# Performance work log

Hardware: AMD Instinct MI355X
Metric: run time of the kernel (lower is better)

The kernel has to match this reference:

```python
import jax, jax.numpy as jnp
import numpy as np

NUM_TEAMS = 200000
EMBED_DIM = 16
NUM_EDGES = 3200000
BATCH = 500000
EPS_NORM = 1e-12  # F.normalize clamp
EPS_SOFTMAX = 1e-16  # PyG edge-softmax denom eps
NEG_SLOPE = 0.01  # LeakyReLU default


def setup_inputs() -> dict:
    key = jax.random.key(0)
    ks = jax.random.split(key, 12)
    inp = {}
    inp["embed"] = jax.random.normal(ks[0], (NUM_TEAMS, EMBED_DIM), dtype=jnp.float32)
    inp["beta"] = jnp.ones((2,), dtype=jnp.float32)  # one learnable scalar per AGNNConv
    # torch Linear init ~ U(-1/sqrt(fan_in), 1/sqrt(fan_in)); stored as [in, out]
    def lin(k, fi, fo):
        b = 1.0 / np.sqrt(fi)
        k1, k2 = jax.random.split(k)
        return (jax.random.uniform(k1, (fi, fo), jnp.float32, -b, b),
                jax.random.uniform(k2, (fo,), jnp.float32, -b, b))
    inp["lin0_w"], inp["lin0_b"] = lin(ks[1], 2 * EMBED_DIM, 6)
    inp["lin1_w"], inp["lin1_b"] = lin(ks[2], 6, 16)
    inp["lin2_w"], inp["lin2_b"] = lin(ks[3], 16, 3)
    inp["edge_index"] = jax.random.randint(ks[4], (2, NUM_EDGES), 0, NUM_TEAMS, dtype=jnp.int64)
    inp["home"] = jax.random.randint(ks[5], (BATCH,), 0, NUM_TEAMS, dtype=jnp.int64)
    inp["away"] = jax.random.randint(ks[6], (BATCH,), 0, NUM_TEAMS, dtype=jnp.int64)
    return inp


def _agnn_conv(x, beta, src, dst, n):
    # x: [N, D]; messages flow src(j) -> dst(i); scatter-softmax over edges per dst
    xn = x / jnp.maximum(jnp.linalg.norm(x, axis=-1, keepdims=True), EPS_NORM)
    alpha = beta * jnp.sum(xn[src] * xn[dst], axis=-1)          # [E]
    m = jax.ops.segment_max(alpha, dst, num_segments=n)          # [N]
    a = jnp.exp(alpha - m[dst])                                   # [E]
    denom = jax.ops.segment_sum(a, dst, num_segments=n)          # [N]
    a = a / (denom[dst] + EPS_SOFTMAX)
    return jax.ops.segment_sum(a[:, None] * x[src], dst, num_segments=n)  # [N, D]


def _forward(embed, beta, lin0_w, lin0_b, lin1_w, lin1_b, lin2_w, lin2_b,
             src, dst, home, away):
    n = embed.shape[0]
    act = lambda v: jax.nn.leaky_relu(v, NEG_SLOPE)
    x = embed  # embedding of arange(n_teams) == the table itself
    x = act(_agnn_conv(x, beta[0], src, dst, n))
    x = act(_agnn_conv(x, beta[1], src, dst, n))
    h = jnp.concatenate([x[home], x[away]], axis=-1)  # [B, 2D]
    h = act(h @ lin0_w + lin0_b)
    h = act(h @ lin1_w + lin1_b)
    h = act(h @ lin2_w + lin2_b)
    return jax.nn.log_softmax(h, axis=0).reshape(-1, 3)  # LogSoftmax(dim=0), faithful


def reference(embed, beta, lin0_w, lin0_b, lin1_w, lin1_b, lin2_w, lin2_b,
              edge_index, home, away):
    n = embed.shape[0]
    # AGNNConv default: remove then add self-loops
    loops = jnp.arange(n, dtype=edge_index.dtype)
    mask = edge_index[0] != edge_index[1]
    safe = jnp.where(mask, edge_index[1], edge_index[0])  # self-loop-out non-loop edges
    src = jnp.concatenate([edge_index[0], loops])
    dst = jnp.concatenate([jnp.where(mask, edge_index[1], edge_index[0]), loops])
    # masked self-loops in original list become src==dst duplicates of the appended
    # self-loops only if random collision; to faithfully *remove* them we redirect
    # removed edges onto the node's own appended self-loop (alpha identical for
    # src==dst), which changes only duplicate self-loop counts with prob ~1/N.
    return _forward(embed, beta, lin0_w, lin0_b, lin1_w, lin1_b, lin2_w, lin2_b,
                    src, dst, home, away)
```

## Files before the change

### kernel.cpp

```cpp
#include <hip/hip_runtime.h>
#include <hip/hip_fp16.h>
#include <math.h>

#define TPB 256
#define NPB 512
#define NPB_SHIFT 9
#define EPB 8192
#define EPW 16
#define BCAP 12288

typedef float v2f __attribute__((ext_vector_type(2)));

__device__ __forceinline__ float leaky_relu(float v) { return v > 0.0f ? v : 0.01f * v; }

__device__ __forceinline__ float dot4(float4 a, float4 b) {
    return a.x * b.x + a.y * b.y + a.z * b.z + a.w * b.w;
}
__device__ __forceinline__ float4 f4_scale(float4 a, float s) {
    return make_float4(a.x * s, a.y * s, a.z * s, a.w * s);
}
__device__ __forceinline__ float4 f4_acc(float4 a, float w, float4 y) {
    return make_float4(fmaf(w, y.x, a.x), fmaf(w, y.y, a.y),
                       fmaf(w, y.z, a.z), fmaf(w, y.w, a.w));
}
__device__ __forceinline__ float4 f4_add_shfl(float4 v, int d) {
    return make_float4(v.x + __shfl_xor(v.x, d, 64), v.y + __shfl_xor(v.y, d, 64),
                       v.z + __shfl_xor(v.z, d, 64), v.w + __shfl_xor(v.w, d, 64));
}
__device__ __forceinline__ float4 leaky4(float4 v) {
    return make_float4(leaky_relu(v.x), leaky_relu(v.y), leaky_relu(v.z), leaky_relu(v.w));
}

__device__ __forceinline__ float4 dec4(unsigned w) {
    v2f lo = __builtin_amdgcn_cvt_pk_f32_fp8((int)w, false);
    v2f hi = __builtin_amdgcn_cvt_pk_f32_fp8((int)w, true);
    return make_float4(lo.x, lo.y, hi.x, hi.y);
}
__device__ __forceinline__ unsigned enc4(float4 v) {
    int r = __builtin_amdgcn_cvt_pk_fp8_f32(v.x, v.y, 0, false);
    r = __builtin_amdgcn_cvt_pk_fp8_f32(v.z, v.w, r, true);
    return (unsigned)r;
}

__device__ __forceinline__ void store_h4(__half* row, int l, float4 v) {
    union { float2 f; __half h[4]; } u;
    u.h[0] = __float2half(v.x); u.h[1] = __float2half(v.y);
    u.h[2] = __float2half(v.z); u.h[3] = __float2half(v.w);
    ((float2*)row)[l] = u.f;
}

__device__ __forceinline__ int wave_incl_scan(int v, int lane) {
#pragma unroll
    for (int off = 1; off < 64; off <<= 1) {
        int u = __shfl_up(v, off, 64);
        if (lane >= off) v += u;
    }
    return v;
}

__global__ void k_binA(const int* __restrict__ src, const int* __restrict__ dst,
                       unsigned* __restrict__ bdata, int* __restrict__ cbase,
                       int* __restrict__ ccnt, int E, int K,
                       const float* __restrict__ x, uint4* __restrict__ xq,
                       int N) {
    __shared__ int hist[512];
    __shared__ unsigned lcol[EPB];
    __shared__ int wsum[8];
    int t = threadIdx.x;
    int lane = t & 63, wv = t >> 6;
    int c = blockIdx.x;
    int e0 = c * EPB;
    int e1 = min(e0 + EPB, E);
    int tot = e1 - e0;
    hist[t] = 0;
    __syncthreads();
    int myd[EPW], mys[EPW];
    if (tot == EPB) {
        const int4* d4 = (const int4*)(dst + e0);
        const int4* s4 = (const int4*)(src + e0);
#pragma unroll
        for (int k = 0; k < 4; ++k) {
            int4 dd = d4[t + k * 512];
            int4 ss = s4[t + k * 512];
            myd[4 * k + 0] = dd.x; myd[4 * k + 1] = dd.y;
            myd[4 * k + 2] = dd.z; myd[4 * k + 3] = dd.w;
            mys[4 * k + 0] = ss.x; mys[4 * k + 1] = ss.y;
            mys[4 * k + 2] = ss.z; mys[4 * k + 3] = ss.w;
            atomicAdd(&hist[dd.x >> NPB_SHIFT], 1);
            atomicAdd(&hist[dd.y >> NPB_SHIFT], 1);
            atomicAdd(&hist[dd.z >> NPB_SHIFT], 1);
            atomicAdd(&hist[dd.w >> NPB_SHIFT], 1);
        }
    } else {
#pragma unroll
        for (int k = 0; k < EPW; ++k) {
            int e = e0 + t + k * 512;
            int d = (e < e1) ? dst[e] : -1;
            mys[k] = (e < e1) ? src[e] : 0;
            myd[k] = d;
            if (d >= 0) atomicAdd(&hist[d >> NPB_SHIFT], 1);
        }
    }
    __syncthreads();
    int v = hist[t];
    int inc = wave_incl_scan(v, lane);
    if (lane == 63) wsum[wv] = inc;
    __syncthreads();
    if (t == 0) {
        int acc = 0;
#pragma unroll
        for (int k = 0; k < 8; ++k) { int xv = wsum[k]; wsum[k] = acc; acc += xv; }
    }
    __syncthreads();
    int excl = inc + wsum[wv] - v;
    if (t < K) {
        cbase[(size_t)c * K + t] = excl;
        ccnt[(size_t)c * K + t] = v;
    }
    __syncthreads();
    hist[t] = excl;
    __syncthreads();
    if (tot == EPB) {
#pragma unroll
        for (int k = 0; k < EPW; ++k) {
            int d = myd[k];
            int p = atomicAdd(&hist[d >> NPB_SHIFT], 1);
            lcol[p] = ((unsigned)(d & (NPB - 1)) << 18) | (unsigned)mys[k];
        }
    } else {
#pragma unroll
        for (int k = 0; k < EPW; ++k) {
            int d = myd[k];
            if (d >= 0) {
                int p = atomicAdd(&hist[d >> NPB_SHIFT], 1);
                lcol[p] = ((unsigned)(d & (NPB - 1)) << 18) | (unsigned)mys[k];
            }
        }
    }
    __syncthreads();
    unsigned* outp = bdata + (size_t)c * EPB;
    for (int i = t; i < tot; i += 512) outp[i] = lcol[i];
    int i = c * 512 + t;
    if (i < N) {
        const float4* xp = (const float4*)(x + (size_t)i * 16);
        float4 a = xp[0], b = xp[1], cc = xp[2], d = xp[3];
        xq[i] = make_uint4(enc4(a), enc4(b), enc4(cc), enc4(d));
    }
}

__global__ void k_binB(const unsigned* __restrict__ bdata, const int* __restrict__ cbase,
                       const int* __restrict__ ccnt,
                       int2* __restrict__ rng,
                       int* __restrict__ col, int N, int NC, int K) {
    __shared__ int cb[512];
    __shared__ int cc[512];
    __shared__ int ldeg[NPB];
    __shared__ int wsum[8];
    int b = blockIdx.x, t = threadIdx.x;
    int lane = t & 63, wv = t >> 6;
    int n0 = b << NPB_SHIFT;
    int nn = min(NPB, N - n0);
    cb[t] = (t < NC) ? cbase[(size_t)t * K + b] : 0;
    cc[t] = (t < NC) ? ccnt[(size_t)t * K + b] : 0;
    ldeg[t] = 0;
    __syncthreads();
    int mycnt = (t < NC) ? cc[t] : 0;
    const unsigned* myp = bdata + (size_t)t * EPB + cb[t];
    for (int k = 0; k < mycnt; ++k) {
        unsigned e = myp[k];
        atomicAdd(&ldeg[e >> 18], 1);
    }
    __syncthreads();
    int dv = ldeg[t];
    int inc = wave_incl_scan(dv, lane);
    if (lane == 63) wsum[wv] = inc;
    __syncthreads();
    if (t == 0) {
        int acc = 0;
#pragma unroll
        for (int k = 0; k < 8; ++k) { int xv = wsum[k]; wsum[k] = acc; acc += xv; }
    }
    __syncthreads();
    int excl = inc + wsum[wv] - dv;
    int gb = b * BCAP;
    if (t < nn) {
        rng[n0 + t] = make_int2(gb + excl, gb + excl + dv);
    }
    __syncthreads();
    ldeg[t] = excl;
    __syncthreads();
    for (int k = 0; k < mycnt; ++k) {
        unsigned e = myp[k];
        int pos = atomicAdd(&ldeg[e >> 18], 1);
        col[gb + pos] = (int)(e & 0x3FFFFu);
    }
}

__global__ void k_agnn(const uint4* __restrict__ xq,
                       const int2* __restrict__ rng,
                       const int* __restrict__ col,
                       const float* __restrict__ beta_ptr, int beta_idx,
                       void* __restrict__ out, int n, int fp8_out) {
    int t = threadIdx.x;
    int l = t & 7;
    int i = blockIdx.x * (512 / 8) + (t >> 3);
    if (i >= n) return;
    float bet = beta_ptr[beta_idx];
    uint4 rowi = xq[i];
    float4 x0 = dec4(rowi.x), x1 = dec4(rowi.y), x2 = dec4(rowi.z), x3 = dec4(rowi.w);
    float sqi = dot4(x0, x0) + dot4(x1, x1) + dot4(x2, x2) + dot4(x3, x3);
    float inv_ni = rsqrtf(fmaxf(sqi, 1e-24f));
    float bi = bet * inv_ni;
    float4 q0 = f4_scale(x0, bi), q1 = f4_scale(x1, bi),
           q2 = f4_scale(x2, bi), q3 = f4_scale(x3, bi);
    float s;
    float4 a0, a1, a2, a3;
    if (l == 0) {
        float w = __expf(bet);
        s = w;
        a0 = f4_scale(x0, w); a1 = f4_scale(x1, w);
        a2 = f4_scale(x2, w); a3 = f4_scale(x3, w);
    } else {
        s = 0.0f;
        a0 = a1 = a2 = a3 = make_float4(0.f, 0.f, 0.f, 0.f);
    }
    int2 se = rng[i];
    int e1 = se.y;
    int last = max(e1 - 1, 0);
    int e = se.x + l;
    int j0 = min(max(col[min(e, last)], 0), n - 1);
    uint4 rA = xq[j0];
    int j1 = min(max(col[min(e + 8, last)], 0), n - 1);
    uint4 rB = xq[j1];
    for (; e < e1; e += 8) {
        int j2 = min(max(col[min(e + 16, last)], 0), n - 1);
        uint4 rC = xq[j2];
        float4 y0 = dec4(rA.x), y1 = dec4(rA.y), y2 = dec4(rA.z), y3 = dec4(rA.w);
        float sq = dot4(y0, y0) + dot4(y1, y1) + dot4(y2, y2) + dot4(y3, y3);
        float inv_n = rsqrtf(fmaxf(sq, 1e-24f));
        float d = (dot4(y0, q0) + dot4(y1, q1) + dot4(y2, q2) + dot4(y3, q3)) * inv_n;
        float w = __expf(d);
        s += w;
        a0 = f4_acc(a0, w, y0);
        a1 = f4_acc(a1, w, y1);
        a2 = f4_acc(a2, w, y2);
        a3 = f4_acc(a3, w, y3);
        rA = rB; rB = rC;
    }
#pragma unroll
    for (int d_ = 1; d_ < 8; d_ <<= 1) {
        s += __shfl_xor(s, d_, 64);
        a0 = f4_add_shfl(a0, d_);
        a1 = f4_add_shfl(a1, d_);
        a2 = f4_add_shfl(a2, d_);
        a3 = f4_add_shfl(a3, d_);
    }
    float inv = 1.0f / (s + 1e-16f);
    float4 o0 = leaky4(f4_scale(a0, inv));
    float4 o1 = leaky4(f4_scale(a1, inv));
    float4 o2 = leaky4(f4_scale(a2, inv));
    float4 o3 = leaky4(f4_scale(a3, inv));
    if (l < 4) {
        float4 oq = (l == 0) ? o0 : (l == 1) ? o1 : (l == 2) ? o2 : o3;
        if (fp8_out) {
            ((unsigned*)((uint4*)out + i))[l] = enc4(oq);
        } else {
            store_h4((__half*)out + (size_t)i * 16, l, oq);
        }
    }
}

__global__ void k_mlp(const __half* __restrict__ x, const int* __restrict__ home,
                      const int* __restrict__ away,
                      const float* __restrict__ w0, const float* __restrict__ b0,
                      const float* __restrict__ w1, const float* __restrict__ b1,
                      const float* __restrict__ w2, const float* __restrict__ b2,
                      float* __restrict__ z, float* __restrict__ bmax,
                      float* __restrict__ bsum, int nb) {
    __shared__ float sw0[192], sw1[96], sw2[48], sb0[6], sb1[16], sb2[3];
    __shared__ float rmax[4][3];
    __shared__ float rsum[4][3];
    int t = threadIdx.x;
    if (t < 192) sw0[t] = w0[t];
    if (t < 96)  sw1[t] = w1[t];
    if (t < 48)  sw2[t] = w2[t];
    if (t < 6)   sb0[t] = b0[t];
    if (t < 16)  sb1[t] = b1[t];
    if (t < 3)   sb2[t] = b2[t];
    __syncthreads();
    int i = blockIdx.x * blockDim.x + t;
    bool act = i < nb;
    float z0 = -3.4e38f, z1 = -3.4e38f, z2 = -3.4e38f;
    if (act) {
        float h[32];
        const uint4* hr = (const uint4*)(x + (size_t)home[i] * 16);
        const uint4* ar = (const uint4*)(x + (size_t)away[i] * 16);
        uint4 hv0 = hr[0], hv1 = hr[1];
        uint4 av0 = ar[0], av1 = ar[1];
        union { uint4 u; __half2 h2[4]; } cv;
#pragma unroll
        for (int q = 0; q < 4; ++q) {
            cv.u = (q == 0) ? hv0 : (q == 1) ? hv1 : (q == 2) ? av0 : av1;
#pragma unroll
            for (int k = 0; k < 4; ++k) {
                float2 f = __half22float2(cv.h2[k]);
                h[q * 8 + 2 * k + 0] = f.x;
                h[q * 8 + 2 * k + 1] = f.y;
            }
        }
        float t0[6];
#pragma unroll
        for (int o = 0; o < 6; ++o) {
            float acc = sb0[o];
#pragma unroll
            for (int k = 0; k < 32; ++k) acc = fmaf(h[k], sw0[k * 6 + o], acc);
            t0[o] = leaky_relu(acc);
        }
        float t1[16];
#pragma unroll
        for (int o = 0; o < 16; ++o) {
            float acc = sb1[o];
#pragma unroll
            for (int k = 0; k < 6; ++k) acc = fmaf(t0[k], sw1[k * 16 + o], acc);
            t1[o] = leaky_relu(acc);
        }
        float zz[3];
#pragma unroll
        for (int o = 0; o < 3; ++o) {
            float acc = sb2[o];
#pragma unroll
            for (int k = 0; k < 16; ++k) acc = fmaf(t1[k], sw2[k * 3 + o], acc);
            zz[o] = leaky_relu(acc);
            z[(size_t)i * 3 + o] = zz[o];
        }
        z0 = zz[0]; z1 = zz[1]; z2 = zz[2];
    }
    float w0_ = z0, w1_ = z1, w2_ = z2;
#pragma unroll
    for (int off = 32; off > 0; off >>= 1) {
        w0_ = fmaxf(w0_, __shfl_down(w0_, off));
        w1_ = fmaxf(w1_, __shfl_down(w1_, off));
        w2_ = fmaxf(w2_, __shfl_down(w2_, off));
    }
    int wid = t >> 6;
    if ((t & 63) == 0) { rmax[wid][0] = w0_; rmax[wid][1] = w1_; rmax[wid][2] = w2_; }
    __syncthreads();
    float M0 = fmaxf(fmaxf(rmax[0][0], rmax[1][0]), fmaxf(rmax[2][0], rmax[3][0]));
    float M1 = fmaxf(fmaxf(rmax[0][1], rmax[1][1]), fmaxf(rmax[2][1], rmax[3][1]));
    float M2 = fmaxf(fmaxf(rmax[0][2], rmax[1][2]), fmaxf(rmax[2][2], rmax[3][2]));
    float e0 = act ? __expf(z0 - M0) : 0.0f;
    float e1 = act ? __expf(z1 - M1) : 0.0f;
    float e2 = act ? __expf(z2 - M2) : 0.0f;
#pragma unroll
    for (int off = 32; off > 0; off >>= 1) {
        e0 += __shfl_down(e0, off);
        e1 += __shfl_down(e1, off);
        e2 += __shfl_down(e2, off);
    }
    if ((t & 63) == 0) { rsum[wid][0] = e0; rsum[wid][1] = e1; rsum[wid][2] = e2; }
    __syncthreads();
    if (t == 0) {
        float S0 = rsum[0][0] + rsum[1][0] + rsum[2][0] + rsum[3][0];
        float S1 = rsum[0][1] + rsum[1][1] + rsum[2][1] + rsum[3][1];
        float S2 = rsum[0][2] + rsum[1][2] + rsum[2][2] + rsum[3][2];
        bmax[blockIdx.x * 3 + 0] = M0; bmax[blockIdx.x * 3 + 1] = M1; bmax[blockIdx.x * 3 + 2] = M2;
        bsum[blockIdx.x * 3 + 0] = S0; bsum[blockIdx.x * 3 + 1] = S1; bsum[blockIdx.x * 3 + 2] = S2;
    }
}

__device__ __forceinline__ float pick3(int c, float L0, float L1, float L2) {
    return c == 0 ? L0 : (c == 1 ? L1 : L2);
}

__global__ void k_final(const float4* __restrict__ z4,
                        const float* __restrict__ bmax, const float* __restrict__ bsum,
                        int nblk, float4* __restrict__ out4, int n4) {
    __shared__ float lm[4][3];
    __shared__ float ls[4][3];
    __shared__ float Lsh[3];
    int t = threadIdx.x;
    float M0 = -3.4e38f, M1 = -3.4e38f, M2 = -3.4e38f;
    float S0 = 0.f, S1 = 0.f, S2 = 0.f;
    for (int b = t; b < nblk; b += 256) {
        float m0 = bmax[b * 3 + 0], s0 = bsum[b * 3 + 0];
        float n0 = fmaxf(M0, m0); S0 = S0 * __expf(M0 - n0) + s0 * __expf(m0 - n0); M0 = n0;
        float m1 = bmax[b * 3 + 1], s1 = bsum[b * 3 + 1];
        float n1 = fmaxf(M1, m1); S1 = S1 * __expf(M1 - n1) + s1 * __expf(m1 - n1); M1 = n1;
        float m2 = bmax[b * 3 + 2], s2 = bsum[b * 3 + 2];
        float n2 = fmaxf(M2, m2); S2 = S2 * __expf(M2 - n2) + s2 * __expf(m2 - n2); M2 = n2;
    }
#pragma unroll
    for (int off = 32; off > 0; off >>= 1) {
        float mo, so, nm;
        mo = __shfl_down(M0, off); so = __shfl_down(S0, off);
        nm = fmaxf(M0, mo); S0 = S0 * __expf(M0 - nm) + so * __expf(mo - nm); M0 = nm;
        mo = __shfl_down(M1, off); so = __shfl_down(S1, off);
        nm = fmaxf(M1, mo); S1 = S1 * __expf(M1 - nm) + so * __expf(mo - nm); M1 = nm;
        mo = __shfl_down(M2, off); so = __shfl_down(S2, off);
        nm = fmaxf(M2, mo); S2 = S2 * __expf(M2 - nm) + so * __expf(mo - nm); M2 = nm;
    }
    int wid = t >> 6;
    if ((t & 63) == 0) {
        lm[wid][0] = M0; lm[wid][1] = M1; lm[wid][2] = M2;
        ls[wid][0] = S0; ls[wid][1] = S1; ls[wid][2] = S2;
    }
    __syncthreads();
    if (t == 0) {
        for (int w = 1; w < 4; ++w) {
            float nm;
            nm = fmaxf(M0, lm[w][0]); S0 = S0 * __expf(M0 - nm) + ls[w][0] * __expf(lm[w][0] - nm); M0 = nm;
            nm = fmaxf(M1, lm[w][1]); S1 = S1 * __expf(M1 - nm) + ls[w][1] * __expf(lm[w][1] - nm); M1 = nm;
            nm = fmaxf(M2, lm[w][2]); S2 = S2 * __expf(M2 - nm) + ls[w][2] * __expf(lm[w][2] - nm); M2 = nm;
        }
        Lsh[0] = M0 + logf(S0);
        Lsh[1] = M1 + logf(S1);
        Lsh[2] = M2 + logf(S2);
    }
    __syncthreads();
    float L0 = Lsh[0], L1 = Lsh[1], L2 = Lsh[2];
    int i = blockIdx.x * blockDim.x + t;
    if (i >= n4) return;
    float4 v = z4[i];
    int c = i % 3;
    int c1 = (c + 1) % 3, c2 = (c + 2) % 3;
    out4[i] = make_float4(v.x - pick3(c, L0, L1, L2),
                          v.y - pick3(c1, L0, L1, L2),
                          v.z - pick3(c2, L0, L1, L2),
                          v.w - pick3(c, L0, L1, L2));
}

extern "C" void kernel_launch(void* const* d_in, const int* in_sizes, int n_in,
                              void* d_out, int out_size, void* d_ws, size_t ws_size,
                              hipStream_t stream) {
    const float* embed = (const float*)d_in[0];
    const float* beta  = (const float*)d_in[1];
    const float* w0 = (const float*)d_in[2];
    const float* b0 = (const float*)d_in[3];
    const float* w1 = (const float*)d_in[4];
    const float* b1 = (const float*)d_in[5];
    const float* w2 = (const float*)d_in[6];
    const float* b2 = (const float*)d_in[7];
    const int* eidx = (const int*)d_in[8];
    const int* home = (const int*)d_in[9];
    const int* away = (const int*)d_in[10];

    const int N = in_sizes[0] / 16;
    const int E = in_sizes[8] / 2;
    const int B = in_sizes[9];
    const int* esrc = eidx;
    const int* edst = eidx + E;
    const int K = (N + NPB - 1) >> NPB_SHIFT;
    const int NC = (E + EPB - 1) / EPB;

    char* ws = (char*)d_ws;
    size_t off = 0;
    auto alloc = [&](size_t bytes) -> char* {
        off = (off + 255) & ~(size_t)255;
        char* p = ws + off;
        off += bytes;
        return p;
    };
    size_t bdata_bytes = (size_t)NC * EPB * 4;
    size_t alias_bytes = (((size_t)N * 16 + 511) & ~(size_t)255) + (size_t)B * 3 * 4;
    char* U = alloc(bdata_bytes > alias_bytes ? bdata_bytes : alias_bytes);
    unsigned* bdata = (unsigned*)U;
    uint4* xq1  = (uint4*)U;
    float* zbuf = (float*)(U + (((size_t)N * 16 + 511) & ~(size_t)255));

    int2* rng    = (int2*)alloc((size_t)N * 8);
    int* colw    = (int*)alloc((size_t)K * BCAP * 4);
    int* cbase   = (int*)alloc((size_t)NC * K * 4);
    int* ccnt    = (int*)alloc((size_t)NC * K * 4);
    uint4* xq0   = (uint4*)alloc((size_t)N * 16);
    __half* xh2  = (__half*)alloc((size_t)N * 32);
    const int nblkB = (B + TPB - 1) / TPB;
    float* bmax  = (float*)alloc((size_t)nblkB * 3 * 4);
    float* bsum  = (float*)alloc((size_t)nblkB * 3 * 4);
    (void)ws_size; (void)n_in; (void)out_size;

    k_binA<<<NC, 512, 0, stream>>>(esrc, edst, bdata, cbase, ccnt, E, K,
                                   embed, xq0, N);
    k_binB<<<K, 512, 0, stream>>>(bdata, cbase, ccnt, rng, colw, N, NC, K);

    const int nblkN8 = (N + 63) / 64;
    k_agnn<<<nblkN8, 512, 0, stream>>>(xq0, rng, colw, beta, 0, xq1, N, 1);
    k_agnn<<<nblkN8, 512, 0, stream>>>(xq1, rng, colw, beta, 1, xh2, N, 0);

    k_mlp<<<nblkB, TPB, 0, stream>>>(xh2, home, away, w0, b0, w1, b1, w2, b2,
                                     zbuf, bmax, bsum, B);
    const int n4 = (B * 3) / 4;
    k_final<<<(n4 + TPB - 1) / TPB, TPB, 0, stream>>>((const float4*)zbuf, bmax, bsum,
                                                      nblkB, (float4*)d_out, n4);
}
```

Before: 214.3 us.

## Coalesce bin-B reads per chunk and stage sorted columns in LDS

```diff
diff --git a/kernel.cpp b/kernel.cpp
--- a/kernel.cpp
+++ b/kernel.cpp
@@ -62,7 +62,7 @@
                        unsigned* __restrict__ bdata, int* __restrict__ cbase,
                        int* __restrict__ ccnt, int E, int K,
                        const float* __restrict__ x, uint4* __restrict__ xq,
-                       int N) {
+                       int N, int NC) {
     __shared__ int hist[512];
     __shared__ unsigned lcol[EPB];
     __shared__ int wsum[8];
@@ -114,8 +114,8 @@
     __syncthreads();
     int excl = inc + wsum[wv] - v;
     if (t < K) {
-        cbase[(size_t)c * K + t] = excl;
-        ccnt[(size_t)c * K + t] = v;
+        cbase[(size_t)t * NC + c] = excl;
+        ccnt[(size_t)t * NC + c] = v;
     }
     __syncthreads();
     hist[t] = excl;
@@ -152,27 +152,21 @@
                        const int* __restrict__ ccnt,
                        int2* __restrict__ rng,
                        int* __restrict__ col, int N, int NC, int K) {
-    __shared__ int cb[512];
-    __shared__ int cc[512];
+    __shared__ int cb_s[512];
+    __shared__ int cc_s[512];
     __shared__ int ldeg[NPB];
     __shared__ int wsum[8];
+    __shared__ int tot_s;
+    __shared__ int sorted[BCAP];
     int b = blockIdx.x, t = threadIdx.x;
     int lane = t & 63, wv = t >> 6;
     int n0 = b << NPB_SHIFT;
     int nn = min(NPB, N - n0);
-    cb[t] = (t < NC) ? cbase[(size_t)t * K + b] : 0;
-    cc[t] = (t < NC) ? ccnt[(size_t)t * K + b] : 0;
+    int myc = (t < NC) ? ccnt[(size_t)b * NC + t] : 0;
+    cb_s[t] = (t < NC) ? cbase[(size_t)b * NC + t] : 0;
+    cc_s[t] = myc;
     ldeg[t] = 0;
-    __syncthreads();
-    int mycnt = (t < NC) ? cc[t] : 0;
-    const unsigned* myp = bdata + (size_t)t * EPB + cb[t];
-    for (int k = 0; k < mycnt; ++k) {
-        unsigned e = myp[k];
-        atomicAdd(&ldeg[e >> 18], 1);
-    }
-    __syncthreads();
-    int dv = ldeg[t];
-    int inc = wave_incl_scan(dv, lane);
+    int inc = wave_incl_scan(myc, lane);
     if (lane == 63) wsum[wv] = inc;
     __syncthreads();
     if (t == 0) {
@@ -181,19 +175,48 @@
         for (int k = 0; k < 8; ++k) { int xv = wsum[k]; wsum[k] = acc; acc += xv; }
     }
     __syncthreads();
-    int excl = inc + wsum[wv] - dv;
+    int cpref = inc + wsum[wv] - myc;
+    if (t == 511) tot_s = cpref + myc;
+    __syncthreads();
+    int cnt = tot_s;
+    for (int r = 0; r < 64; ++r) {
+        int tt = (wv << 6) + r;
+        int len = cc_s[tt];
+        if (len == 0) continue;
+        const unsigned* sp = bdata + (size_t)tt * EPB + cb_s[tt];
+        for (int k = lane; k < len; k += 64)
+            atomicAdd(&ldeg[sp[k] >> 18], 1);
+    }
+    __syncthreads();
+    int dv = ldeg[t];
+    int inc2 = wave_incl_scan(dv, lane);
+    if (lane == 63) wsum[wv] = inc2;
+    __syncthreads();
+    if (t == 0) {
+        int acc = 0;
+#pragma unroll
+        for (int k = 0; k < 8; ++k) { int xv = wsum[k]; wsum[k] = acc; acc += xv; }
+    }
+    __syncthreads();
+    int excl = inc2 + wsum[wv] - dv;
     int gb = b * BCAP;
-    if (t < nn) {
-        rng[n0 + t] = make_int2(gb + excl, gb + excl + dv);
-    }
+    if (t < nn) rng[n0 + t] = make_int2(gb + excl, gb + excl + dv);
     __syncthreads();
     ldeg[t] = excl;
     __syncthreads();
-    for (int k = 0; k < mycnt; ++k) {
-        unsigned e = myp[k];
-        int pos = atomicAdd(&ldeg[e >> 18], 1);
-        col[gb + pos] = (int)(e & 0x3FFFFu);
-    }
+    for (int r = 0; r < 64; ++r) {
+        int tt = (wv << 6) + r;
+        int len = cc_s[tt];
+        if (len == 0) continue;
+        const unsigned* sp = bdata + (size_t)tt * EPB + cb_s[tt];
+        for (int k = lane; k < len; k += 64) {
+            unsigned tag = sp[k];
+            int pos = atomicAdd(&ldeg[tag >> 18], 1);
+            sorted[pos] = (int)(tag & 0x3FFFFu);
+        }
+    }
+    __syncthreads();
+    for (int i = t; i < cnt; i += 512) col[gb + i] = sorted[i];
 }
 
 __global__ void k_agnn(const uint4* __restrict__ xq,
@@ -479,7 +502,7 @@
     (void)ws_size; (void)n_in; (void)out_size;
 
     k_binA<<<NC, 512, 0, stream>>>(esrc, edst, bdata, cbase, ccnt, E, K,
-                                   embed, xq0, N);
+                                   embed, xq0, N, NC);
     k_binB<<<K, 512, 0, stream>>>(bdata, cbase, ccnt, rng, colw, N, NC, K);
 
     const int nblkN8 = (N + 63) / 64;
```

Measured after the change: 240.0 us. +12.0%, slower.
